# Kernel optimization log

Hardware: AMD Instinct MI355X
Metric: run time of the kernel (lower is better)

## Reference

```python
import jax, jax.numpy as jnp
import numpy as np

# TT factorization of a 4096 -> 4096 linear layer
IN_SHAPE = (8, 8, 8, 8)    # input_tt_shape, prod = 4096
OUT_SHAPE = (8, 8, 8, 8)   # output_tt_shape, prod = 4096
RANKS = (1, 16, 16, 16, 1) # tt_ranks, len = n_dim + 1
N_DIM = len(IN_SHAPE)
BATCH = 2048
OUT_SIZE = int(np.prod(OUT_SHAPE))
IN_SIZE = int(np.prod(IN_SHAPE))


def setup_inputs() -> dict:
    key = jax.random.key(0)
    ks = jax.random.split(key, N_DIM + 1)
    x = jax.random.normal(ks[0], (BATCH, IN_SIZE), dtype=jnp.float32)
    inp = {"x": x}
    for i in range(N_DIM):
        rows = RANKS[i] * OUT_SHAPE[i]
        cols = IN_SHAPE[i] * RANKS[i + 1]
        # xavier_uniform scale, matching torch init statistics
        limit = float(np.sqrt(6.0 / (rows + cols)))
        inp[f"core{i}"] = jax.random.uniform(
            ks[i + 1], (rows, cols), minval=-limit, maxval=limit, dtype=jnp.float32
        )
    inp["bias"] = jnp.zeros((OUT_SIZE,), dtype=jnp.float32)
    return inp


def reference(x, core0, core1, core2, core3, bias):
    cores = [core0, core1, core2, core3]
    res = x  # [B, prod(IN_SHAPE)]
    # Sequential TT-core contraction, last mode first (faithful to torch loop)
    for k in range(N_DIM - 1, -1, -1):
        res = res.reshape(-1, IN_SHAPE[k])                     # [.., n_k]
        res = res.T                                            # [n_k, ..]
        res = res.reshape(RANKS[k + 1] * IN_SHAPE[k], -1)      # [r_{k+1}*n_k, ..]
        res = cores[k] @ res                                   # [r_k*m_k, ..]
    res = res.reshape(OUT_SIZE, -1).T                          # [B, prod(OUT_SHAPE)]
    return res + bias
```

## Files before the change

### kernel.cpp

```cpp
#include <hip/hip_runtime.h>
#include <hip/hip_bf16.h>
#include <stdint.h>


typedef __bf16 bf16_t;
typedef __bf16 bf16x8 __attribute__((ext_vector_type(8)));
typedef float floatx4 __attribute__((ext_vector_type(4)));

#define BATCH_N 2048
#define KD 4096
#define ND 4096

__device__ static inline void load_lds16(const void* g, void* l) {
    __builtin_amdgcn_global_load_lds(
        (const __attribute__((address_space(1))) void*)g,
        (__attribute__((address_space(3))) void*)l, 16, 0, 0);
}

__global__ __launch_bounds__(256) void cvt_x(const float* __restrict__ x,
                                             bf16_t* __restrict__ xb) {
    int t = blockIdx.x * 256 + threadIdx.x;
    const float4* xv = (const float4*)x;
    float4 a = xv[t * 2];
    float4 b = xv[t * 2 + 1];
    bf16x8 o;
    o[0] = (bf16_t)a.x; o[1] = (bf16_t)a.y; o[2] = (bf16_t)a.z; o[3] = (bf16_t)a.w;
    o[4] = (bf16_t)b.x; o[5] = (bf16_t)b.y; o[6] = (bf16_t)b.z; o[7] = (bf16_t)b.w;
    ((bf16x8*)xb)[t] = o;
}

__global__ __launch_bounds__(256) void build_w(const float* __restrict__ c0,
                                               const float* __restrict__ c1,
                                               const float* __restrict__ c2,
                                               const float* __restrict__ c3,
                                               bf16_t* __restrict__ W) {
    __shared__ float c0s[8 * 16];
    __shared__ float c1s[16 * 8 * 16];
    __shared__ float c2s[16 * 8 * 16];
    __shared__ float c3s[16 * 8];
    __shared__ float Ps[64 * 16];
    __shared__ float T1s[16 * 64];
    const int b = blockIdx.x;
    const int M23 = b >> 6, N01 = b & 63;
    const int n0 = N01 >> 3, n1 = N01 & 7, m2 = M23 >> 3, m3 = M23 & 7;
    const int t = threadIdx.x;

    if (t < 128) c0s[t] = c0[(t >> 4) * 128 + n0 * 16 + (t & 15)];
    if (t < 128) c3s[t] = c3[((t >> 3) * 8 + m3) * 8 + (t & 7)];
    for (int i = t; i < 2048; i += 256) {
        int r1 = i >> 7, m1 = (i >> 4) & 7, r2 = i & 15;
        c1s[i] = c1[(r1 * 8 + m1) * 128 + n1 * 16 + r2];
    }
    for (int i = t; i < 2048; i += 256) {
        int r2 = i >> 7, n2 = (i >> 4) & 7, r3 = i & 15;
        c2s[i] = c2[(r2 * 8 + m2) * 128 + n2 * 16 + r3];
    }
    __syncthreads();

    for (int i = t; i < 1024; i += 256) {
        int m01 = i >> 4, r2 = i & 15, m0 = m01 >> 3, m1 = m01 & 7;
        float s = 0.f;
#pragma unroll
        for (int r1 = 0; r1 < 16; ++r1)
            s += c0s[m0 * 16 + r1] * c1s[r1 * 128 + m1 * 16 + r2];
        Ps[i] = s;
    }
    for (int i = t; i < 1024; i += 256) {
        int r2 = i >> 6, n23 = i & 63, n2 = n23 >> 3, n3 = n23 & 7;
        float s = 0.f;
#pragma unroll
        for (int r3 = 0; r3 < 16; ++r3)
            s += c2s[r2 * 128 + n2 * 16 + r3] * c3s[r3 * 8 + n3];
        T1s[i] = s;
    }
    __syncthreads();

    const int n23 = t & 63, q = t >> 6;
#pragma unroll
    for (int g = 0; g < 16; ++g) {
        int m01 = q * 16 + g;
        float s = 0.f;
#pragma unroll
        for (int r2 = 0; r2 < 16; ++r2) s += Ps[m01 * 16 + r2] * T1s[r2 * 64 + n23];
        W[(size_t)(m01 * 64 + M23) * 4096 + N01 * 64 + n23] = (bf16_t)s;
    }
}

__global__ __launch_bounds__(256) void gemm_bt(const bf16_t* __restrict__ A,
                                               const bf16_t* __restrict__ B,
                                               const float* __restrict__ bias,
                                               float* __restrict__ C) {
    __shared__ bf16_t As[64 * 32];
    __shared__ bf16_t Bs[128 * 32];
    const int t = threadIdx.x;
    const int bn = blockIdx.x, bm = blockIdx.y;
    const int lane = t & 63, wave = t >> 6;
    const int wm = wave >> 1, wn = wave & 1;

    const int sr = t >> 2;
    const int sk = ((t & 3) ^ ((t >> 3) & 3)) * 8;
    const bf16_t* Agp = A + (size_t)(bm * 64 + sr) * KD + sk;
    const bf16_t* Bgp = B + (size_t)(bn * 128 + sr) * KD + sk;
    bf16_t* AsW = As + wave * 512;
    bf16_t* BsW0 = Bs + wave * 512;
    bf16_t* BsW1 = Bs + 2048 + wave * 512;

    floatx4 acc[2][4];
    floatx4 zero = {0.f, 0.f, 0.f, 0.f};
#pragma unroll
    for (int i = 0; i < 2; ++i)
#pragma unroll
        for (int j = 0; j < 4; ++j) acc[i][j] = zero;

    const int fr = lane & 15;
    const int pk = ((lane >> 4) ^ ((lane >> 1) & 3)) * 8;

    for (int k0 = 0; k0 < KD; k0 += 32) {
        __syncthreads();
        load_lds16(Agp + k0, AsW);
        load_lds16(Bgp + k0, BsW0);
        load_lds16(Bgp + (size_t)64 * KD + k0, BsW1);
        __syncthreads();

        bf16x8 af[2], bf[4];
#pragma unroll
        for (int im = 0; im < 2; ++im)
            af[im] = *(const bf16x8*)(As + (wm * 32 + im * 16 + fr) * 32 + pk);
#pragma unroll
        for (int in = 0; in < 4; ++in)
            bf[in] = *(const bf16x8*)(Bs + (wn * 64 + in * 16 + fr) * 32 + pk);
#pragma unroll
        for (int im = 0; im < 2; ++im)
#pragma unroll
            for (int in = 0; in < 4; ++in)
                acc[im][in] = __builtin_amdgcn_mfma_f32_16x16x32_bf16(
                    af[im], bf[in], acc[im][in], 0, 0, 0);
    }

    const int rl = lane >> 4, cl = lane & 15;
    const size_t rbase = (size_t)bm * 64 + wm * 32;
    const int cbase = bn * 128 + wn * 64;
#pragma unroll
    for (int im = 0; im < 2; ++im) {
#pragma unroll
        for (int in = 0; in < 4; ++in) {
            int col = cbase + in * 16 + cl;
            float bv = bias[col];
#pragma unroll
            for (int r = 0; r < 4; ++r) {
                size_t row = rbase + im * 16 + rl * 4 + r;
                C[row * ND + col] = acc[im][in][r] + bv;
            }
        }
    }
}

extern "C" void kernel_launch(void* const* d_in, const int* in_sizes, int n_in,
                              void* d_out, int out_size, void* d_ws, size_t ws_size,
                              hipStream_t stream) {
    const float* x  = (const float*)d_in[0];
    const float* c0 = (const float*)d_in[1];
    const float* c1 = (const float*)d_in[2];
    const float* c2 = (const float*)d_in[3];
    const float* c3 = (const float*)d_in[4];
    const float* bias = (const float*)d_in[5];
    float* out = (float*)d_out;

    char* ws = (char*)d_ws;
    bf16_t* Xb = (bf16_t*)ws;
    bf16_t* W  = (bf16_t*)(ws + (16u << 20));

    cvt_x<<<4096, 256, 0, stream>>>(x, Xb);
    build_w<<<4096, 256, 0, stream>>>(c0, c1, c2, c3, W);
    dim3 grid(ND / 128, BATCH_N / 64);
    gemm_bt<<<grid, 256, 0, stream>>>(Xb, W, bias, out);
}
```

Before: 210.8 us.

## Enlarge GEMM tile to 128x128 with K-step 64 and new LDS swizzle

```diff
diff --git a/kernel.cpp b/kernel.cpp
--- a/kernel.cpp
+++ b/kernel.cpp
@@ -86,62 +86,67 @@
     }
 }
 
-__global__ __launch_bounds__(256) void gemm_bt(const bf16_t* __restrict__ A,
-                                               const bf16_t* __restrict__ B,
-                                               const float* __restrict__ bias,
-                                               float* __restrict__ C) {
-    __shared__ bf16_t As[64 * 32];
-    __shared__ bf16_t Bs[128 * 32];
+__global__ __launch_bounds__(256, 2) void gemm_bt(const bf16_t* __restrict__ A,
+                                                  const bf16_t* __restrict__ B,
+                                                  const float* __restrict__ bias,
+                                                  float* __restrict__ C) {
+    __shared__ bf16_t As[128 * 64];
+    __shared__ bf16_t Bs[128 * 64];
     const int t = threadIdx.x;
     const int bn = blockIdx.x, bm = blockIdx.y;
     const int lane = t & 63, wave = t >> 6;
     const int wm = wave >> 1, wn = wave & 1;
 
-    const int sr = t >> 2;
-    const int sk = ((t & 3) ^ ((t >> 3) & 3)) * 8;
-    const bf16_t* Agp = A + (size_t)(bm * 64 + sr) * KD + sk;
-    const bf16_t* Bgp = B + (size_t)(bn * 128 + sr) * KD + sk;
+    const int srow = lane >> 3;
+    const int lc = (lane & 7) ^ srow;
+    const bf16_t* Agp = A + (size_t)(bm * 128 + wave * 8 + srow) * KD + lc * 8;
+    const bf16_t* Bgp = B + (size_t)(bn * 128 + wave * 8 + srow) * KD + lc * 8;
     bf16_t* AsW = As + wave * 512;
-    bf16_t* BsW0 = Bs + wave * 512;
-    bf16_t* BsW1 = Bs + 2048 + wave * 512;
+    bf16_t* BsW = Bs + wave * 512;
 
-    floatx4 acc[2][4];
+    floatx4 acc[4][4];
     floatx4 zero = {0.f, 0.f, 0.f, 0.f};
 #pragma unroll
-    for (int i = 0; i < 2; ++i)
+    for (int i = 0; i < 4; ++i)
 #pragma unroll
         for (int j = 0; j < 4; ++j) acc[i][j] = zero;
 
     const int fr = lane & 15;
-    const int pk = ((lane >> 4) ^ ((lane >> 1) & 3)) * 8;
+    const int fc = lane >> 4;
 
-    for (int k0 = 0; k0 < KD; k0 += 32) {
+    for (int k0 = 0; k0 < KD; k0 += 64) {
         __syncthreads();
-        load_lds16(Agp + k0, AsW);
-        load_lds16(Bgp + k0, BsW0);
-        load_lds16(Bgp + (size_t)64 * KD + k0, BsW1);
+#pragma unroll
+        for (int j = 0; j < 4; ++j) {
+            load_lds16(Agp + (size_t)(j * 32) * KD + k0, AsW + j * 2048);
+            load_lds16(Bgp + (size_t)(j * 32) * KD + k0, BsW + j * 2048);
+        }
         __syncthreads();
 
-        bf16x8 af[2], bf[4];
 #pragma unroll
-        for (int im = 0; im < 2; ++im)
-            af[im] = *(const bf16x8*)(As + (wm * 32 + im * 16 + fr) * 32 + pk);
+        for (int kk = 0; kk < 2; ++kk) {
+            const int pA = (fc + kk * 4) ^ (fr & 7);
+            bf16x8 af[4], bf[4];
 #pragma unroll
-        for (int in = 0; in < 4; ++in)
-            bf[in] = *(const bf16x8*)(Bs + (wn * 64 + in * 16 + fr) * 32 + pk);
-#pragma unroll
-        for (int im = 0; im < 2; ++im)
+            for (int im = 0; im < 4; ++im)
+                af[im] = *(const bf16x8*)(As + (wm * 64 + im * 16 + fr) * 64 + pA * 8);
 #pragma unroll
             for (int in = 0; in < 4; ++in)
-                acc[im][in] = __builtin_amdgcn_mfma_f32_16x16x32_bf16(
-                    af[im], bf[in], acc[im][in], 0, 0, 0);
+                bf[in] = *(const bf16x8*)(Bs + (wn * 64 + in * 16 + fr) * 64 + pA * 8);
+#pragma unroll
+            for (int im = 0; im < 4; ++im)
+#pragma unroll
+                for (int in = 0; in < 4; ++in)
+                    acc[im][in] = __builtin_amdgcn_mfma_f32_16x16x32_bf16(
+                        af[im], bf[in], acc[im][in], 0, 0, 0);
+        }
     }
 
     const int rl = lane >> 4, cl = lane & 15;
-    const size_t rbase = (size_t)bm * 64 + wm * 32;
+    const size_t rbase = (size_t)bm * 128 + wm * 64;
     const int cbase = bn * 128 + wn * 64;
 #pragma unroll
-    for (int im = 0; im < 2; ++im) {
+    for (int im = 0; im < 4; ++im) {
 #pragma unroll
         for (int in = 0; in < 4; ++in) {
             int col = cbase + in * 16 + cl;
@@ -172,6 +177,6 @@
 
     cvt_x<<<4096, 256, 0, stream>>>(x, Xb);
     build_w<<<4096, 256, 0, stream>>>(c0, c1, c2, c3, W);
-    dim3 grid(ND / 128, BATCH_N / 64);
+    dim3 grid(ND / 128, BATCH_N / 128);
     gemm_bt<<<grid, 256, 0, stream>>>(Xb, W, bias, out);
 }
```

Measured after the change: 183.2 us. 13.1% less time.
